# Performance work log

Measured on AMD Instinct MI355X. Metric: run time of the kernel, lower is better.

The kernel has to match this reference:

```python
import jax, jax.numpy as jnp
import numpy as np

D_OUT, D1, D2 = 512, 512, 512
R0, R1, R2 = 128, 128, 128
BATCH = 8192


def setup_inputs() -> dict:
    key = jax.random.key(0)
    k1, k2, k3, k4, k5, k6 = jax.random.split(key, 6)
    return {
        "X1": jax.random.normal(k1, (D1, BATCH), dtype=jnp.float32),
        "X2": jax.random.normal(k2, (D2, BATCH), dtype=jnp.float32),
        "U0": jax.random.normal(k3, (D_OUT, R0), dtype=jnp.float32) * 0.05,
        "U1": jax.random.normal(k4, (D1, R1), dtype=jnp.float32) * 0.05,
        "U2": jax.random.normal(k5, (D2, R2), dtype=jnp.float32) * 0.05,
        "G": jax.random.normal(k6, (R0, R1, R2), dtype=jnp.float32) * 0.05,
    }


def reference(X1, X2, U0, U1, U2, G):
    # Per-mode projections: UX_i = U_{i+1}^T @ X_i  -> [r_i, B]
    UX1 = U1.T @ X1  # [R1, B]
    UX2 = U2.T @ X2  # [R2, B]
    # Column-wise Khatri-Rao product of UX1, UX2 gives kron per column with
    # row index q*R2 + r (C order), which matches mode-0 unfolding of G.
    # Fused form: core = G_(0) @ khatri_rao(UX1, UX2), expressed as one einsum.
    core = jnp.einsum('pqr,qb,rb->pb', G, UX1, UX2)  # [R0, B]
    Z = U0 @ core  # [D_OUT, B]
    return Z
```

## Files before the change

kernel.cpp:

```cpp
#include <hip/hip_runtime.h>
#include <hip/hip_bf16.h>
#include <stdint.h>


typedef __attribute__((ext_vector_type(8))) short bf8;
typedef __attribute__((ext_vector_type(4))) short bf4;
typedef __attribute__((ext_vector_type(4))) float f4;

__device__ __forceinline__ unsigned short f2bf(float f){
  unsigned x = __builtin_bit_cast(unsigned, f);
  x += 0x7fffu + ((x >> 16) & 1u);
  return (unsigned short)(x >> 16);
}
__device__ __forceinline__ float bf2f(unsigned short u){
  unsigned x = ((unsigned)u) << 16;
  return __builtin_bit_cast(float, x);
}
__device__ __forceinline__ void glds16(const void* g, void* l){
  __builtin_amdgcn_global_load_lds(
      (const __attribute__((address_space(1))) void*)g,
      (__attribute__((address_space(3))) void*)l, 16, 0, 0);
}

__global__ __launch_bounds__(256) void k_castG(const float* __restrict__ G,
                                               const float* __restrict__ U0,
                                               unsigned short* __restrict__ Gbf,
                                               unsigned short* __restrict__ U0bf){
  const int i4 = blockIdx.x * 256 + threadIdx.x;
  const int NG4 = 2097152 / 4;
  const float4* src; unsigned short* dst; int j4;
  if (i4 < NG4){ src = (const float4*)G;  dst = Gbf;  j4 = i4; }
  else         { src = (const float4*)U0; dst = U0bf; j4 = i4 - NG4; }
  float4 v = src[j4];
  ushort4 o = make_ushort4(f2bf(v.x), f2bf(v.y), f2bf(v.z), f2bf(v.w));
  ((ushort4*)dst)[j4] = o;
}

__global__ __launch_bounds__(256) void k_castUT(const float* __restrict__ U1,
                                                const float* __restrict__ U2,
                                                unsigned short* __restrict__ U1T,
                                                unsigned short* __restrict__ U2T){
  const int blk = blockIdx.x;
  const float* U = (blk < 256) ? U1 : U2;
  unsigned short* UT = (blk < 256) ? U1T : U2T;
  const int idx = (blk & 255) * 256 + threadIdx.x;
  const int d = idx >> 7, q = idx & 127;
  UT[q * 512 + d] = f2bf(U[idx]);
}

__global__ __launch_bounds__(256) void k_ux2(const unsigned short* __restrict__ U1T,
                                             const unsigned short* __restrict__ U2T,
                                             const float* __restrict__ X1,
                                             const float* __restrict__ X2,
                                             float* __restrict__ OUTF,
                                             unsigned short* __restrict__ OUTT){
  const bool second = (blockIdx.y != 0);
  const unsigned short* UT = second ? U2T : U1T;
  const float* X = second ? X2 : X1;
  __shared__ __align__(16) unsigned char lds[16384 + 8192];
  unsigned char* ldsA = lds;
  unsigned char* ldsB = lds + 16384;
  const int tid = threadIdx.x, lane = tid & 63, wv = tid >> 6;
  const int wr = wv >> 1, wc = wv & 1;
  const int b0 = blockIdx.x * 64;
  f4 acc[4][2] = {};

  for (int it = 0; it < 8; ++it){
    const int k0 = it * 64;
#pragma unroll
    for (int i = 0; i < 4; ++i){
      const int L = (wv * 4 + i) * 1024 + lane * 16;
      const int row = L >> 7;
      const int ss = (lane & 7) ^ (row & 7);
      glds16(UT + (size_t)row * 512 + k0 + ss * 8, ldsA + (wv * 4 + i) * 1024);
    }
#pragma unroll
    for (int c = 0; c < 2; ++c){
      const int slot = c * 4 + wv;
      const int bRow = lane;
      bf8 v;
#pragma unroll
      for (int j = 0; j < 8; ++j)
        v[j] = (short)f2bf(X[(size_t)(k0 + slot * 8 + j) * 8192 + b0 + bRow]);
      *(bf8*)(ldsB + bRow * 128 + ((slot ^ (bRow & 7)) << 4)) = v;
    }
    __syncthreads();
#pragma unroll
    for (int kc = 0; kc < 2; ++kc){
      const int g = lane >> 4;
      bf8 a[4], b[2];
#pragma unroll
      for (int mf = 0; mf < 4; ++mf){
        const int r = wr * 64 + mf * 16 + (lane & 15);
        a[mf] = *(const bf8*)(ldsA + r * 128 + (((kc * 4 + g) ^ (r & 7)) << 4));
      }
#pragma unroll
      for (int nf = 0; nf < 2; ++nf){
        const int rb = wc * 32 + nf * 16 + (lane & 15);
        b[nf] = *(const bf8*)(ldsB + rb * 128 + (((kc * 4 + g) ^ (rb & 7)) << 4));
      }
#pragma unroll
      for (int mf = 0; mf < 4; ++mf)
#pragma unroll
        for (int nf = 0; nf < 2; ++nf)
          acc[mf][nf] = __builtin_amdgcn_mfma_f32_16x16x32_bf16(a[mf], b[nf], acc[mf][nf], 0, 0, 0);
    }
    __syncthreads();
  }

  if (!second){
#pragma unroll
    for (int mf = 0; mf < 4; ++mf)
#pragma unroll
      for (int nf = 0; nf < 2; ++nf)
#pragma unroll
        for (int j = 0; j < 4; ++j){
          const int q = wr * 64 + mf * 16 + (lane >> 4) * 4 + j;
          const int b = b0 + wc * 32 + nf * 16 + (lane & 15);
          OUTF[(size_t)q * 8192 + b] = acc[mf][nf][j];
        }
  } else {
#pragma unroll
    for (int mf = 0; mf < 4; ++mf)
#pragma unroll
      for (int nf = 0; nf < 2; ++nf){
        const int rBase = wr * 64 + mf * 16 + (lane >> 4) * 4;
        const int bL = wc * 32 + nf * 16 + (lane & 15);
        bf4 p;
#pragma unroll
        for (int j = 0; j < 4; ++j) p[j] = (short)f2bf(acc[mf][nf][j]);
        *(bf4*)(lds + ((bL * 256 + rBase * 2) ^ ((bL & 7) << 4))) = p;
      }
    __syncthreads();
#pragma unroll
    for (int u = 0; u < 4; ++u){
      const int sIdx = u * 256 + tid;
      const int bL = sIdx >> 4, slot = sIdx & 15;
      bf8 v = *(const bf8*)(lds + bL * 256 + ((slot ^ (bL & 7)) << 4));
      *(bf8*)(OUTT + (size_t)(b0 + bL) * 128 + slot * 8) = v;
    }
  }
}

__global__ __launch_bounds__(512, 2) void k_core(const unsigned short* __restrict__ Gbf,
                                                 const float* __restrict__ UX1,
                                                 const unsigned short* __restrict__ UX2T,
                                                 float* __restrict__ PT){
  __shared__ __align__(16) unsigned char lds[98304];
  unsigned char* ldsB = lds + 65536;
  const int tid = threadIdx.x, lane = tid & 63, wv = tid >> 6;
  const int wr = wv >> 2, wc = wv & 3;
  const int b0 = blockIdx.x * 128;
  const int split = blockIdx.y;
  const int g = lane >> 4, l15 = lane & 15;

#pragma unroll
  for (int h = 0; h < 2; ++h)
#pragma unroll
    for (int rnd = 0; rnd < 2; ++rnd){
      const int off = rnd * 8192 + wv * 1024 + lane * 16;
      const int row = off >> 7;
      const int ss = (lane & 7) ^ (row & 7);
      glds16(UX2T + (size_t)(b0 + row) * 128 + h * 64 + ss * 8,
             ldsB + h * 16384 + off);
    }

  const int q0 = split * 32;
#pragma unroll
  for (int h = 0; h < 2; ++h)
#pragma unroll
    for (int rnd = 0; rnd < 2; ++rnd){
      const int off = rnd * 8192 + wv * 1024 + lane * 16;
      const int row = off >> 7;
      const int ss = (lane & 7) ^ (row & 7);
      glds16(Gbf + (size_t)row * 16384 + q0 * 128 + h * 64 + ss * 8,
             lds + h * 16384 + off);
    }
  __syncthreads();

  bf8 bfr[4][2];
#pragma unroll
  for (int kc = 0; kc < 4; ++kc)
#pragma unroll
    for (int nf = 0; nf < 2; ++nf){
      const int rb = wc * 32 + nf * 16 + l15;
      bfr[kc][nf] = *(const bf8*)(ldsB + (kc >> 1) * 16384 + rb * 128 +
                                  ((((kc & 1) * 4 + g) ^ (rb & 7)) << 4));
    }

  f4 acc[4][2] = {};
  int buf = 0;
  for (int i = 0; i < 32; ++i){
    const int q = q0 + i;
    if (i + 1 < 32){
#pragma unroll
      for (int h = 0; h < 2; ++h)
#pragma unroll
        for (int rnd = 0; rnd < 2; ++rnd){
          const int off = rnd * 8192 + wv * 1024 + lane * 16;
          const int row = off >> 7;
          const int ss = (lane & 7) ^ (row & 7);
          glds16(Gbf + (size_t)row * 16384 + (q + 1) * 128 + h * 64 + ss * 8,
                 lds + (buf ^ 1) * 32768 + h * 16384 + off);
        }
    }
    float x1v[2];
#pragma unroll
    for (int nf = 0; nf < 2; ++nf)
      x1v[nf] = UX1[(size_t)q * 8192 + b0 + wc * 32 + nf * 16 + l15];

    const unsigned char* A = lds + buf * 32768;
    f4 y[4][2];
#pragma unroll
    for (int kc = 0; kc < 4; ++kc){
      bf8 a[4];
#pragma unroll
      for (int mf = 0; mf < 4; ++mf){
        const int r = wr * 64 + mf * 16 + l15;
        a[mf] = *(const bf8*)(A + (kc >> 1) * 16384 + r * 128 +
                              ((((kc & 1) * 4 + g) ^ (r & 7)) << 4));
      }
#pragma unroll
      for (int mf = 0; mf < 4; ++mf)
#pragma unroll
        for (int nf = 0; nf < 2; ++nf){
          f4 c = (kc == 0) ? (f4){0.f, 0.f, 0.f, 0.f} : y[mf][nf];
          y[mf][nf] = __builtin_amdgcn_mfma_f32_16x16x32_bf16(a[mf], bfr[kc][nf], c, 0, 0, 0);
        }
    }
#pragma unroll
    for (int mf = 0; mf < 4; ++mf)
#pragma unroll
      for (int nf = 0; nf < 2; ++nf)
        acc[mf][nf] += y[mf][nf] * x1v[nf];
    __syncthreads();
    buf ^= 1;
  }

#pragma unroll
  for (int mf = 0; mf < 4; ++mf)
#pragma unroll
    for (int nf = 0; nf < 2; ++nf){
      const int pq = wr * 16 + mf * 4 + g;
      const int bL = wc * 32 + nf * 16 + l15;
      *(f4*)(lds + bL * 512 + ((pq ^ (bL & 7)) << 4)) = acc[mf][nf];
    }
  __syncthreads();
#pragma unroll
  for (int rnd = 0; rnd < 8; ++rnd){
    const int idx = rnd * 512 + tid;
    const int bL = idx >> 5, sl = idx & 31;
    f4 v = *(const f4*)(lds + bL * 512 + ((sl ^ (bL & 7)) << 4));
    *(f4*)(PT + (size_t)split * 1048576 + (size_t)(b0 + bL) * 128 + sl * 4) = v;
  }
}

__global__ __launch_bounds__(256) void k_red(const float* __restrict__ PT,
                                             unsigned short* __restrict__ coreT){
  const int i4 = blockIdx.x * 256 + threadIdx.x;
  const f4* P = (const f4*)PT;
  f4 v = P[i4];
  v += P[262144 + i4];
  v += P[2 * 262144 + i4];
  v += P[3 * 262144 + i4];
  ushort4 o = make_ushort4(f2bf(v[0]), f2bf(v[1]), f2bf(v[2]), f2bf(v[3]));
  ((ushort4*)coreT)[i4] = o;
}

__global__ __launch_bounds__(256) void k_z(const unsigned short* __restrict__ U0bf,
                                           const unsigned short* __restrict__ coreT,
                                           float* __restrict__ Z){
  __shared__ __align__(16) unsigned char lds[32768];
  unsigned char* ldsA = lds;
  unsigned char* ldsB = lds + 16384;
  const int tid = threadIdx.x, lane = tid & 63, wv = tid >> 6;
  const int wr = wv >> 1, wc = wv & 1;
  const int b0 = blockIdx.x * 128;
  const int d0 = blockIdx.y * 128;
  f4 acc[4][4] = {};

#pragma unroll
  for (int it = 0; it < 2; ++it){
    const int k0 = it * 64;
#pragma unroll
    for (int i = 0; i < 4; ++i){
      const int L = (wv * 4 + i) * 1024 + lane * 16;
      const int row = L >> 7;
      const int ss = (lane & 7) ^ (row & 7);
      glds16(U0bf + (size_t)(d0 + row) * 128 + k0 + ss * 8, ldsA + (wv * 4 + i) * 1024);
      glds16(coreT + (size_t)(b0 + row) * 128 + k0 + ss * 8, ldsB + (wv * 4 + i) * 1024);
    }
    __syncthreads();
#pragma unroll
    for (int kc = 0; kc < 2; ++kc){
      const int g = lane >> 4;
      bf8 a[4], b[4];
#pragma unroll
      for (int mf = 0; mf < 4; ++mf){
        const int r = wr * 64 + mf * 16 + (lane & 15);
        a[mf] = *(const bf8*)(ldsA + r * 128 + (((kc * 4 + g) ^ (r & 7)) << 4));
      }
#pragma unroll
      for (int nf = 0; nf < 4; ++nf){
        const int rb = wc * 64 + nf * 16 + (lane & 15);
        b[nf] = *(const bf8*)(ldsB + rb * 128 + (((kc * 4 + g) ^ (rb & 7)) << 4));
      }
#pragma unroll
      for (int mf = 0; mf < 4; ++mf)
#pragma unroll
        for (int nf = 0; nf < 4; ++nf)
          acc[mf][nf] = __builtin_amdgcn_mfma_f32_16x16x32_bf16(a[mf], b[nf], acc[mf][nf], 0, 0, 0);
    }
    __syncthreads();
  }
#pragma unroll
  for (int mf = 0; mf < 4; ++mf)
#pragma unroll
    for (int nf = 0; nf < 4; ++nf)
#pragma unroll
      for (int j = 0; j < 4; ++j){
        const int d = d0 + wr * 64 + mf * 16 + (lane >> 4) * 4 + j;
        const int b = b0 + wc * 64 + nf * 16 + (lane & 15);
        Z[(size_t)d * 8192 + b] = acc[mf][nf][j];
      }
}

extern "C" void kernel_launch(void* const* d_in, const int* in_sizes, int n_in,
                              void* d_out, int out_size, void* d_ws, size_t ws_size,
                              hipStream_t stream){
  const float* X1 = (const float*)d_in[0];
  const float* X2 = (const float*)d_in[1];
  const float* U0 = (const float*)d_in[2];
  const float* U1 = (const float*)d_in[3];
  const float* U2 = (const float*)d_in[4];
  const float* G  = (const float*)d_in[5];
  float* Z = (float*)d_out;

  char* ws = (char*)d_ws;
  unsigned short* Gbf   = (unsigned short*)(ws);
  unsigned short* U0bf  = (unsigned short*)(ws + 4194304);
  unsigned short* U1T   = (unsigned short*)(ws + 4325376);
  unsigned short* U2T   = (unsigned short*)(ws + 4456448);
  float*          UX1   = (float*)         (ws + 4587520);
  unsigned short* UX2T  = (unsigned short*)(ws + 8781824);
  unsigned short* coreT = (unsigned short*)(ws + 10878976);
  float*          PT    = (float*)         (ws + 12976128);

  k_castG <<<dim3(2112), dim3(256), 0, stream>>>(G, U0, Gbf, U0bf);
  k_castUT<<<dim3(512),  dim3(256), 0, stream>>>(U1, U2, U1T, U2T);
  k_ux2   <<<dim3(128, 2), dim3(256), 0, stream>>>(U1T, U2T, X1, X2, UX1, UX2T);
  k_core  <<<dim3(64, 4), dim3(512), 0, stream>>>(Gbf, UX1, UX2T, PT);
  k_red   <<<dim3(1024),  dim3(256), 0, stream>>>(PT, coreT);
  k_z     <<<dim3(64, 4), dim3(256), 0, stream>>>(U0bf, coreT, Z);
}
```

Baseline: 71.73 us.

## Restructure core kernel to stream G from global with register-held UX2 fragments

The core contraction kernel no longer stages G and UX2 through LDS with double buffering. Each wave now owns 16 output rows, keeps all UX2 B-fragments in registers per half, and streams G rows and UX1 scalars directly from global memory with one-step register prefetch. Blocks are remapped so that split and batch tiles are assigned by XCD index, which should improve L2 locality of G. The two cast kernels are also merged into one launch. This drops LDS traffic and barriers, at the cost of more register pressure and uncoalesced, latency-exposed global loads for G.

After: 82.16 us, median of 2. 14.5% more time.

```diff
diff --git a/kernel.cpp b/kernel.cpp
--- a/kernel.cpp
+++ b/kernel.cpp
@@ -22,30 +22,32 @@
       (__attribute__((address_space(3))) void*)l, 16, 0, 0);
 }
 
-__global__ __launch_bounds__(256) void k_castG(const float* __restrict__ G,
-                                               const float* __restrict__ U0,
-                                               unsigned short* __restrict__ Gbf,
-                                               unsigned short* __restrict__ U0bf){
-  const int i4 = blockIdx.x * 256 + threadIdx.x;
-  const int NG4 = 2097152 / 4;
-  const float4* src; unsigned short* dst; int j4;
-  if (i4 < NG4){ src = (const float4*)G;  dst = Gbf;  j4 = i4; }
-  else         { src = (const float4*)U0; dst = U0bf; j4 = i4 - NG4; }
-  float4 v = src[j4];
-  ushort4 o = make_ushort4(f2bf(v.x), f2bf(v.y), f2bf(v.z), f2bf(v.w));
-  ((ushort4*)dst)[j4] = o;
-}
-
-__global__ __launch_bounds__(256) void k_castUT(const float* __restrict__ U1,
-                                                const float* __restrict__ U2,
-                                                unsigned short* __restrict__ U1T,
-                                                unsigned short* __restrict__ U2T){
+__global__ __launch_bounds__(256) void k_cast(const float* __restrict__ G,
+                                              const float* __restrict__ U0,
+                                              const float* __restrict__ U1,
+                                              const float* __restrict__ U2,
+                                              unsigned short* __restrict__ Gbf,
+                                              unsigned short* __restrict__ U0bf,
+                                              unsigned short* __restrict__ U1T,
+                                              unsigned short* __restrict__ U2T){
   const int blk = blockIdx.x;
-  const float* U = (blk < 256) ? U1 : U2;
-  unsigned short* UT = (blk < 256) ? U1T : U2T;
-  const int idx = (blk & 255) * 256 + threadIdx.x;
-  const int d = idx >> 7, q = idx & 127;
-  UT[q * 512 + d] = f2bf(U[idx]);
+  if (blk < 2112){
+    const int i4 = blk * 256 + threadIdx.x;
+    const int NG4 = 2097152 / 4;
+    const float4* src; unsigned short* dst; int j4;
+    if (i4 < NG4){ src = (const float4*)G;  dst = Gbf;  j4 = i4; }
+    else         { src = (const float4*)U0; dst = U0bf; j4 = i4 - NG4; }
+    float4 v = src[j4];
+    ushort4 o = make_ushort4(f2bf(v.x), f2bf(v.y), f2bf(v.z), f2bf(v.w));
+    ((ushort4*)dst)[j4] = o;
+  } else {
+    const int b2 = blk - 2112;
+    const float* U = (b2 < 256) ? U1 : U2;
+    unsigned short* UT = (b2 < 256) ? U1T : U2T;
+    const int idx = (b2 & 255) * 256 + threadIdx.x;
+    const int d = idx >> 7, q = idx & 127;
+    UT[q * 512 + d] = f2bf(U[idx]);
+  }
 }
 
 __global__ __launch_bounds__(256) void k_ux2(const unsigned short* __restrict__ U1T,
@@ -146,105 +148,77 @@
                                                  const float* __restrict__ UX1,
                                                  const unsigned short* __restrict__ UX2T,
                                                  float* __restrict__ PT){
-  __shared__ __align__(16) unsigned char lds[98304];
-  unsigned char* ldsB = lds + 65536;
+  __shared__ __align__(16) unsigned char lds[65536];
   const int tid = threadIdx.x, lane = tid & 63, wv = tid >> 6;
-  const int wr = wv >> 2, wc = wv & 3;
-  const int b0 = blockIdx.x * 128;
-  const int split = blockIdx.y;
   const int g = lane >> 4, l15 = lane & 15;
-
-#pragma unroll
-  for (int h = 0; h < 2; ++h)
-#pragma unroll
-    for (int rnd = 0; rnd < 2; ++rnd){
-      const int off = rnd * 8192 + wv * 1024 + lane * 16;
-      const int row = off >> 7;
-      const int ss = (lane & 7) ^ (row & 7);
-      glds16(UX2T + (size_t)(b0 + row) * 128 + h * 64 + ss * 8,
-             ldsB + h * 16384 + off);
-    }
-
+  const int blk = blockIdx.x;
+  const int xcd = blk & 7, slot = blk >> 3;
+  const int split = xcd >> 1;
+  const int bblk = (xcd & 1) * 32 + slot;
+  const int b0 = bblk * 128;
   const int q0 = split * 32;
-#pragma unroll
-  for (int h = 0; h < 2; ++h)
-#pragma unroll
-    for (int rnd = 0; rnd < 2; ++rnd){
-      const int off = rnd * 8192 + wv * 1024 + lane * 16;
-      const int row = off >> 7;
-      const int ss = (lane & 7) ^ (row & 7);
-      glds16(Gbf + (size_t)row * 16384 + q0 * 128 + h * 64 + ss * 8,
-             lds + h * 16384 + off);
-    }
-  __syncthreads();
-
-  bf8 bfr[4][2];
-#pragma unroll
-  for (int kc = 0; kc < 4; ++kc)
-#pragma unroll
-    for (int nf = 0; nf < 2; ++nf){
-      const int rb = wc * 32 + nf * 16 + l15;
-      bfr[kc][nf] = *(const bf8*)(ldsB + (kc >> 1) * 16384 + rb * 128 +
-                                  ((((kc & 1) * 4 + g) ^ (rb & 7)) << 4));
-    }
-
-  f4 acc[4][2] = {};
-  int buf = 0;
-  for (int i = 0; i < 32; ++i){
-    const int q = q0 + i;
-    if (i + 1 < 32){
-#pragma unroll
-      for (int h = 0; h < 2; ++h)
-#pragma unroll
-        for (int rnd = 0; rnd < 2; ++rnd){
-          const int off = rnd * 8192 + wv * 1024 + lane * 16;
-          const int row = off >> 7;
-          const int ss = (lane & 7) ^ (row & 7);
-          glds16(Gbf + (size_t)row * 16384 + (q + 1) * 128 + h * 64 + ss * 8,
-                 lds + (buf ^ 1) * 32768 + h * 16384 + off);
-        }
-    }
-    float x1v[2];
-#pragma unroll
-    for (int nf = 0; nf < 2; ++nf)
-      x1v[nf] = UX1[(size_t)q * 8192 + b0 + wc * 32 + nf * 16 + l15];
-
-    const unsigned char* A = lds + buf * 32768;
-    f4 y[4][2];
-#pragma unroll
-    for (int kc = 0; kc < 4; ++kc){
-      bf8 a[4];
-#pragma unroll
-      for (int mf = 0; mf < 4; ++mf){
-        const int r = wr * 64 + mf * 16 + l15;
-        a[mf] = *(const bf8*)(A + (kc >> 1) * 16384 + r * 128 +
-                              ((((kc & 1) * 4 + g) ^ (r & 7)) << 4));
-      }
-#pragma unroll
-      for (int mf = 0; mf < 4; ++mf)
-#pragma unroll
-        for (int nf = 0; nf < 2; ++nf){
-          f4 c = (kc == 0) ? (f4){0.f, 0.f, 0.f, 0.f} : y[mf][nf];
-          y[mf][nf] = __builtin_amdgcn_mfma_f32_16x16x32_bf16(a[mf], bfr[kc][nf], c, 0, 0, 0);
-        }
-    }
-#pragma unroll
-    for (int mf = 0; mf < 4; ++mf)
-#pragma unroll
-      for (int nf = 0; nf < 2; ++nf)
-        acc[mf][nf] += y[mf][nf] * x1v[nf];
-    __syncthreads();
-    buf ^= 1;
-  }
-
-#pragma unroll
-  for (int mf = 0; mf < 4; ++mf)
-#pragma unroll
-    for (int nf = 0; nf < 2; ++nf){
-      const int pq = wr * 16 + mf * 4 + g;
-      const int bL = wc * 32 + nf * 16 + l15;
-      *(f4*)(lds + bL * 512 + ((pq ^ (bL & 7)) << 4)) = acc[mf][nf];
-    }
+  const int p0 = wv * 16;
+
+  f4 acc[8] = {(f4){0,0,0,0}};
+#pragma unroll
+  for (int nf = 0; nf < 8; ++nf) acc[nf] = (f4){0.f, 0.f, 0.f, 0.f};
+
+#pragma unroll
+  for (int h = 0; h < 2; ++h){
+    bf8 Bf[2][8];
+#pragma unroll
+    for (int kc = 0; kc < 2; ++kc)
+#pragma unroll
+      for (int nf = 0; nf < 8; ++nf)
+        Bf[kc][nf] = *(const bf8*)(UX2T + (size_t)(b0 + nf * 16 + l15) * 128 +
+                                   h * 64 + kc * 32 + g * 8);
+    const unsigned short* ap = Gbf + (size_t)(p0 + l15) * 16384 + q0 * 128 + h * 64 + g * 8;
+    const float* xp = UX1 + (size_t)q0 * 8192 + b0 + l15;
+
+    bf8 a0 = *(const bf8*)(ap);
+    bf8 a1 = *(const bf8*)(ap + 32);
+    float xs[8];
+#pragma unroll
+    for (int nf = 0; nf < 8; ++nf) xs[nf] = xp[nf * 16];
+
+    for (int i = 0; i < 31; ++i){
+      bf8 n0 = *(const bf8*)(ap + (i + 1) * 128);
+      bf8 n1 = *(const bf8*)(ap + (i + 1) * 128 + 32);
+      float xn[8];
+#pragma unroll
+      for (int nf = 0; nf < 8; ++nf) xn[nf] = xp[(size_t)(i + 1) * 8192 + nf * 16];
+      f4 y[8];
+#pragma unroll
+      for (int nf = 0; nf < 8; ++nf)
+        y[nf] = __builtin_amdgcn_mfma_f32_16x16x32_bf16(a0, Bf[0][nf], (f4){0.f,0.f,0.f,0.f}, 0, 0, 0);
+#pragma unroll
+      for (int nf = 0; nf < 8; ++nf)
+        y[nf] = __builtin_amdgcn_mfma_f32_16x16x32_bf16(a1, Bf[1][nf], y[nf], 0, 0, 0);
+#pragma unroll
+      for (int nf = 0; nf < 8; ++nf) acc[nf] += y[nf] * xs[nf];
+      a0 = n0; a1 = n1;
+#pragma unroll
+      for (int nf = 0; nf < 8; ++nf) xs[nf] = xn[nf];
+    }
+    {
+      f4 y[8];
+#pragma unroll
+      for (int nf = 0; nf < 8; ++nf)
+        y[nf] = __builtin_amdgcn_mfma_f32_16x16x32_bf16(a0, Bf[0][nf], (f4){0.f,0.f,0.f,0.f}, 0, 0, 0);
+#pragma unroll
+      for (int nf = 0; nf < 8; ++nf)
+        y[nf] = __builtin_amdgcn_mfma_f32_16x16x32_bf16(a1, Bf[1][nf], y[nf], 0, 0, 0);
+#pragma unroll
+      for (int nf = 0; nf < 8; ++nf) acc[nf] += y[nf] * xs[nf];
+    }
+  }
+
+#pragma unroll
+  for (int nf = 0; nf < 8; ++nf){
+    const int bL = nf * 16 + l15;
+    const int pq = wv * 4 + g;
+    *(f4*)(lds + bL * 512 + ((pq ^ (bL & 7)) << 4)) = acc[nf];
+  }
   __syncthreads();
 #pragma unroll
   for (int rnd = 0; rnd < 8; ++rnd){
@@ -346,10 +320,9 @@
   unsigned short* coreT = (unsigned short*)(ws + 10878976);
   float*          PT    = (float*)         (ws + 12976128);
 
-  k_castG <<<dim3(2112), dim3(256), 0, stream>>>(G, U0, Gbf, U0bf);
-  k_castUT<<<dim3(512),  dim3(256), 0, stream>>>(U1, U2, U1T, U2T);
-  k_ux2   <<<dim3(128, 2), dim3(256), 0, stream>>>(U1T, U2T, X1, X2, UX1, UX2T);
-  k_core  <<<dim3(64, 4), dim3(512), 0, stream>>>(Gbf, UX1, UX2T, PT);
-  k_red   <<<dim3(1024),  dim3(256), 0, stream>>>(PT, coreT);
-  k_z     <<<dim3(64, 4), dim3(256), 0, stream>>>(U0bf, coreT, Z);
-}
+  k_cast<<<dim3(2624), dim3(256), 0, stream>>>(G, U0, U1, U2, Gbf, U0bf, U1T, U2T);
+  k_ux2 <<<dim3(128, 2), dim3(256), 0, stream>>>(U1T, U2T, X1, X2, UX1, UX2T);
+  k_core<<<dim3(256), dim3(512), 0, stream>>>(Gbf, UX1, UX2T, PT);
+  k_red <<<dim3(1024), dim3(256), 0, stream>>>(PT, coreT);
+  k_z   <<<dim3(64, 4), dim3(256), 0, stream>>>(U0bf, coreT, Z);
+}
```
